# Performance work log

Measured on AMD Instinct MI355X. Metric: run time of the kernel, lower is better.

The kernel has to match this reference:

```python
import jax, jax.numpy as jnp
import numpy as np

D = 64      # hiddenDims
DQ = 64     # queryDims
M = 64      # inducingPoints
B = 64      # number of ragged segments
LMAX = 4096 # max segment length
Z = float(np.sqrt(DQ))
EPS = 1e-5


def _segment_lengths():
    rng = np.random.default_rng(0)
    return rng.integers(512, LMAX + 1, size=B)


def setup_inputs() -> dict:
    xl = _segment_lengths()
    total = int(xl.sum())
    key = jax.random.key(0)
    ks = jax.random.split(key, 12)
    s = 0.05
    inp = {
        "x": jax.random.normal(ks[0], (total, D), jnp.float32),
        "xlens": jnp.asarray(xl, jnp.int32),
        "I": jax.random.uniform(ks[1], (M, D), jnp.float32),
        # AttentionBlock 0 (queries = inducing points)
        "WQ0": jax.random.normal(ks[2], (DQ, D), jnp.float32) * s,
        "WK0": jax.random.normal(ks[3], (DQ, D), jnp.float32) * s,
        "WV0": jax.random.normal(ks[4], (D, D), jnp.float32) * s,
        "FCw0": jax.random.normal(ks[5], (D, D), jnp.float32) * s,
        "FCb0": jnp.zeros((D,), jnp.float32),
        "g00": jnp.ones((D,), jnp.float32), "b00": jnp.zeros((D,), jnp.float32),
        "g01": jnp.ones((D,), jnp.float32), "b01": jnp.zeros((D,), jnp.float32),
        # AttentionBlock 1 (queries = tokens)
        "WQ1": jax.random.normal(ks[6], (DQ, D), jnp.float32) * s,
        "WK1": jax.random.normal(ks[7], (DQ, D), jnp.float32) * s,
        "WV1": jax.random.normal(ks[8], (D, D), jnp.float32) * s,
        "FCw1": jax.random.normal(ks[9], (D, D), jnp.float32) * s,
        "FCb1": jnp.zeros((D,), jnp.float32),
        "g10": jnp.ones((D,), jnp.float32), "b10": jnp.zeros((D,), jnp.float32),
        "g11": jnp.ones((D,), jnp.float32), "b11": jnp.zeros((D,), jnp.float32),
    }
    return inp


def _ln(x, g, b):
    m = jnp.mean(x, axis=-1, keepdims=True)
    v = jnp.mean(jnp.square(x - m), axis=-1, keepdims=True)
    return (x - m) * jax.lax.rsqrt(v + EPS) * g + b


def _attn_block(q, h, mask_kv, WQ, WK, WV, FCw, FCb, g0, b0, g1, b1):
    # q: [B,Lq,D], h: [B,Lk,D], mask_kv: [B,Lk] or None
    qq = q @ WQ.T                     # [B,Lq,DQ]
    k = h @ WK.T                      # [B,Lk,DQ]
    v = h @ WV.T                      # [B,Lk,D]
    s = jnp.einsum('bqe,bke->bqk', qq, k) / Z
    if mask_kv is not None:
        s = jnp.where(mask_kv[:, None, :], s, -1e30)
    a = jax.nn.softmax(s, axis=-1)
    hh = _ln(q + jnp.einsum('bqk,bkd->bqd', a, v), g0, b0)
    return _ln(hh + jax.nn.relu(hh @ FCw.T + FCb), g1, b1)


def reference(x, xlens, I,
              WQ0, WK0, WV0, FCw0, FCb0, g00, b00, g01, b01,
              WQ1, WK1, WV1, FCw1, FCb1, g10, b10, g11, b11):
    xl = np.asarray(xlens)
    b_idx = np.concatenate([np.full(int(l), b, np.int32) for b, l in enumerate(xl)])
    pos = np.concatenate([np.arange(int(l), dtype=np.int32) for l in xl])
    mask = jnp.asarray(np.arange(LMAX)[None, :] < xl[:, None])   # [B,LMAX]

    padded = jnp.zeros((B, LMAX, D), x.dtype).at[b_idx, pos].set(x)

    # ab0: queries = inducing points (shared), keys/values = set elements
    q0 = jnp.broadcast_to(I[None], (B, M, D))
    i_seg = _attn_block(q0, padded, mask, WQ0, WK0, WV0, FCw0, FCb0, g00, b00, g01, b01)  # [B,M,D]

    # ab1: queries = set elements, keys/values = induced points
    out = _attn_block(padded, i_seg, None, WQ1, WK1, WV1, FCw1, FCb1, g10, b10, g11, b11)  # [B,LMAX,D]

    return out[b_idx, pos]  # flat ragged output [total, D]
```

## Files before the change

### kernel.cpp

```cpp
#include <hip/hip_runtime.h>

#define NB 64
#define NCHUNK 8
#define NSUB 16
#define ZINV 0.125f
#define EPS 1e-5f

typedef __attribute__((ext_vector_type(8))) short short8;
typedef __attribute__((ext_vector_type(4))) float f32x4;
typedef unsigned short ushort_t;

__device__ __forceinline__ f32x4 mm(short8 a, short8 b, f32x4 c) {
  return __builtin_amdgcn_mfma_f32_16x16x32_bf16(a, b, c, 0, 0, 0);
}
__device__ __forceinline__ ushort_t f2bf(float f) {
  unsigned u = __float_as_uint(f);
  u += 0x7fffu + ((u >> 16) & 1u);
  return (ushort_t)(u >> 16);
}
__device__ __forceinline__ unsigned pack2(float a, float b) {
  return (unsigned)f2bf(a) | ((unsigned)f2bf(b) << 16);
}
__device__ __forceinline__ short8 cvt8(float4 a, float4 b) {
  union { unsigned u[4]; short8 s; } z;
  z.u[0] = pack2(a.x, a.y); z.u[1] = pack2(a.z, a.w);
  z.u[2] = pack2(b.x, b.y); z.u[3] = pack2(b.z, b.w);
  return z.s;
}
__device__ __forceinline__ void cvt16(const float* __restrict__ src, ushort_t* dst) {
  const float4* s = (const float4*)src;
  unsigned* d = (unsigned*)dst;
  float4 A0 = s[0], A1 = s[1], A2 = s[2], A3 = s[3];
  d[0] = pack2(A0.x, A0.y); d[1] = pack2(A0.z, A0.w);
  d[2] = pack2(A1.x, A1.y); d[3] = pack2(A1.z, A1.w);
  d[4] = pack2(A2.x, A2.y); d[5] = pack2(A2.z, A2.w);
  d[6] = pack2(A3.x, A3.y); d[7] = pack2(A3.z, A3.w);
}

__global__ __launch_bounds__(256) void k_setup(const int* __restrict__ xlens,
                                               const float* __restrict__ I,
                                               const float* __restrict__ WQ0,
                                               const float* __restrict__ WK0,
                                               const float* __restrict__ FCw1,
                                               const float* __restrict__ WV0,
                                               const float* __restrict__ FCw0,
                                               const float* __restrict__ WK1,
                                               const float* __restrict__ WQ1,
                                               const float* __restrict__ WV1,
                                               int* __restrict__ off,
                                               ushort_t* __restrict__ QK0bf,
                                               ushort_t* __restrict__ Wfcbf,
                                               ushort_t* __restrict__ WV0bf,
                                               ushort_t* __restrict__ FCw0bf,
                                               ushort_t* __restrict__ WK1bf,
                                               ushort_t* __restrict__ WQ1Tbf,
                                               ushort_t* __restrict__ WV1bf) {
  int tid = threadIdx.x;
  if (tid < 64) {
    int v = xlens[tid];
#pragma unroll
    for (int d = 1; d < 64; d <<= 1) {
      int t = __shfl_up(v, d);
      if (tid >= d) v += t;
    }
    off[tid + 1] = v;
    if (tid == 0) off[0] = 0;
  }
  __shared__ ushort_t Ibf[64][72];
  __shared__ ushort_t Wq0[64][72];
  __shared__ ushort_t Wk0T[64][72];
  __shared__ ushort_t qqbf[64][72];

  int w = tid >> 6, l = tid & 63, l15 = l & 15, lh = l >> 4;
  int srow = tid >> 2, sc0 = (tid & 3) << 4;
  int so = srow * 64 + sc0;

  cvt16(I + so, &Ibf[srow][sc0]);
  cvt16(WQ0 + so, &Wq0[srow][sc0]);
  {
    const float* s = WK0 + so;
#pragma unroll
    for (int i = 0; i < 16; ++i) Wk0T[sc0 + i][srow] = f2bf(s[i]);
  }
  cvt16(FCw1 + so, Wfcbf + so);
  cvt16(WV0 + so, WV0bf + so);
  cvt16(FCw0 + so, FCw0bf + so);
  cvt16(WK1 + so, WK1bf + so);
  cvt16(WV1 + so, WV1bf + so);
  {
    const float* s = WQ1 + so;
#pragma unroll
    for (int i = 0; i < 16; ++i) WQ1Tbf[(sc0 + i) * 64 + srow] = f2bf(s[i]);
  }
  __syncthreads();

  short8 ai0 = *(const short8*)&Ibf[16 * w + l15][lh * 8];
  short8 ai1 = *(const short8*)&Ibf[16 * w + l15][32 + lh * 8];
  f32x4 cA[4];
#pragma unroll
  for (int n = 0; n < 4; ++n) {
    short8 b0 = *(const short8*)&Wq0[16 * n + l15][lh * 8];
    short8 b1 = *(const short8*)&Wq0[16 * n + l15][32 + lh * 8];
    cA[n] = mm(ai0, b0, (f32x4){0.f, 0.f, 0.f, 0.f});
    cA[n] = mm(ai1, b1, cA[n]);
  }
#pragma unroll
  for (int n = 0; n < 4; ++n)
#pragma unroll
    for (int r = 0; r < 4; ++r)
      qqbf[16 * w + 4 * lh + r][16 * n + l15] = f2bf(cA[n][r]);

  short8 aq0 = *(const short8*)&qqbf[16 * w + l15][lh * 8];
  short8 aq1 = *(const short8*)&qqbf[16 * w + l15][32 + lh * 8];
  f32x4 cB[4];
#pragma unroll
  for (int n = 0; n < 4; ++n) {
    short8 b0 = *(const short8*)&Wk0T[16 * n + l15][lh * 8];
    short8 b1 = *(const short8*)&Wk0T[16 * n + l15][32 + lh * 8];
    cB[n] = mm(aq0, b0, (f32x4){0.f, 0.f, 0.f, 0.f});
    cB[n] = mm(aq1, b1, cB[n]);
  }
#pragma unroll
  for (int n = 0; n < 4; ++n)
#pragma unroll
    for (int r = 0; r < 4; ++r)
      QK0bf[(16 * w + 4 * lh + r) * 64 + 16 * n + l15] = f2bf(cB[n][r] * ZINV);
}

__global__ __launch_bounds__(256) void k_phaseA(const float* __restrict__ x,
                                                const int* __restrict__ off,
                                                const ushort_t* __restrict__ QK0bf,
                                                float* __restrict__ part_sm,
                                                float* __restrict__ part_ax) {
  int b = blockIdx.x / NCHUNK, chunk = blockIdx.x % NCHUNK;
  int s0 = off[b], L = off[b + 1] - s0;
  int clen = (L + NCHUNK - 1) / NCHUNK;
  int t0 = chunk * clen;
  int t1 = t0 + clen; if (t1 > L) t1 = L;

  __shared__ ushort_t xbf[64][72];
  __shared__ ushort_t xT[64][72];
  __shared__ ushort_t pbf[64][72];

  int tid = threadIdx.x;
  int w = tid >> 6, l = tid & 63, l15 = l & 15, lh = l >> 4;
  int srow = tid >> 2, sc0 = (tid & 3) << 4;

  short8 aq0 = *(const short8*)(QK0bf + ((16 * w + l15) << 6) + lh * 8);
  short8 aq1 = *(const short8*)(QK0bf + ((16 * w + l15) << 6) + 32 + lh * 8);

  float sm[4] = {0.f, 0.f, 0.f, 0.f};
  f32x4 acc[4];
#pragma unroll
  for (int n = 0; n < 4; ++n) acc[n] = (f32x4){0.f, 0.f, 0.f, 0.f};

  float4 P0, P1, P2, P3;
  {
    int g = t0 + srow;
    int gc = g < t1 ? g : t1 - 1;
    const float4* src = (const float4*)(x + ((size_t)(s0 + gc) << 6) + sc0);
    P0 = src[0]; P1 = src[1]; P2 = src[2]; P3 = src[3];
  }

  for (int tt = t0; tt < t1; tt += 64) {
    __syncthreads();
    {
      float vv[16] = {P0.x, P0.y, P0.z, P0.w, P1.x, P1.y, P1.z, P1.w,
                      P2.x, P2.y, P2.z, P2.w, P3.x, P3.y, P3.z, P3.w};
      unsigned* dst = (unsigned*)&xbf[srow][sc0];
      dst[0] = pack2(vv[0], vv[1]);   dst[1] = pack2(vv[2], vv[3]);
      dst[2] = pack2(vv[4], vv[5]);   dst[3] = pack2(vv[6], vv[7]);
      dst[4] = pack2(vv[8], vv[9]);   dst[5] = pack2(vv[10], vv[11]);
      dst[6] = pack2(vv[12], vv[13]); dst[7] = pack2(vv[14], vv[15]);
#pragma unroll
      for (int i = 0; i < 16; ++i) xT[sc0 + i][srow] = f2bf(vv[i]);
    }
    __syncthreads();
    if (tt + 64 < t1) {
      int g = tt + 64 + srow;
      int gc = g < t1 ? g : t1 - 1;
      const float4* src = (const float4*)(x + ((size_t)(s0 + gc) << 6) + sc0);
      P0 = src[0]; P1 = src[1]; P2 = src[2]; P3 = src[3];
    }
    f32x4 c1[4];
#pragma unroll
    for (int n = 0; n < 4; ++n) {
      short8 bx0 = *(const short8*)&xbf[16 * n + l15][lh * 8];
      short8 bx1 = *(const short8*)&xbf[16 * n + l15][32 + lh * 8];
      c1[n] = mm(aq0, bx0, (f32x4){0.f, 0.f, 0.f, 0.f});
      c1[n] = mm(aq1, bx1, c1[n]);
    }
#pragma unroll
    for (int n = 0; n < 4; ++n) {
      bool v = (tt + 16 * n + l15) < t1;
#pragma unroll
      for (int r = 0; r < 4; ++r) {
        float pv = v ? __expf(c1[n][r]) : 0.f;
        c1[n][r] = pv;
        sm[r] += pv;
      }
    }
#pragma unroll
    for (int n = 0; n < 4; ++n)
#pragma unroll
      for (int r = 0; r < 4; ++r)
        pbf[16 * w + 4 * lh + r][16 * n + l15] = f2bf(c1[n][r]);
    short8 pa0 = *(const short8*)&pbf[16 * w + l15][lh * 8];
    short8 pa1 = *(const short8*)&pbf[16 * w + l15][32 + lh * 8];
#pragma unroll
    for (int n = 0; n < 4; ++n) {
      short8 bt0 = *(const short8*)&xT[16 * n + l15][lh * 8];
      short8 bt1 = *(const short8*)&xT[16 * n + l15][32 + lh * 8];
      acc[n] = mm(pa0, bt0, acc[n]);
      acc[n] = mm(pa1, bt1, acc[n]);
    }
  }
  int base = (b * NCHUNK + chunk) * 64;
#pragma unroll
  for (int r = 0; r < 4; ++r) {
    sm[r] += __shfl_xor(sm[r], 1);
    sm[r] += __shfl_xor(sm[r], 2);
    sm[r] += __shfl_xor(sm[r], 4);
    sm[r] += __shfl_xor(sm[r], 8);
  }
  if (l15 == 0) {
#pragma unroll
    for (int r = 0; r < 4; ++r)
      part_sm[base + 16 * w + 4 * lh + r] = sm[r];
  }
#pragma unroll
  for (int n = 0; n < 4; ++n)
#pragma unroll
    for (int r = 0; r < 4; ++r) {
      int m = 16 * w + 4 * lh + r;
      part_ax[((size_t)(base + m) << 6) + 16 * n + l15] = acc[n][r];
    }
}

__global__ __launch_bounds__(256) void k_combine(const float* __restrict__ part_sm,
                                                 const float* __restrict__ part_ax,
                                                 const float* __restrict__ I,
                                                 const ushort_t* __restrict__ WV0bf,
                                                 const ushort_t* __restrict__ FCw0bf,
                                                 const float* __restrict__ FCb0,
                                                 const float* __restrict__ g00,
                                                 const float* __restrict__ b00,
                                                 const float* __restrict__ g01,
                                                 const float* __restrict__ b01,
                                                 const ushort_t* __restrict__ WK1bf,
                                                 const ushort_t* __restrict__ WQ1Tbf,
                                                 const ushort_t* __restrict__ WV1bf,
                                                 ushort_t* __restrict__ K1fbf,
                                                 ushort_t* __restrict__ V1Tbf) {
  int b = blockIdx.x;
  int tid = threadIdx.x;
  int w = tid >> 6, l = tid & 63, l15 = l & 15, lh = l >> 4;

  __shared__ ushort_t av[64][72];
  __shared__ ushort_t sb[64][72];

  {
    int m = tid >> 2, dq = tid & 3, e0 = dq << 4;
    float S = 0.f;
    float ax[16];
#pragma unroll
    for (int i = 0; i < 16; ++i) ax[i] = 0.f;
#pragma unroll
    for (int c = 0; c < NCHUNK; ++c) {
      int pb = (b * NCHUNK + c) * 64 + m;
      S += part_sm[pb];
      const f32x4* pa = (const f32x4*)(part_ax + ((size_t)pb << 6) + e0);
#pragma unroll
      for (int qd = 0; qd < 4; ++qd) {
        f32x4 v = pa[qd];
#pragma unroll
        for (int j = 0; j < 4; ++j) ax[qd * 4 + j] += v[j];
      }
    }
    float invS = 1.f / S;
    unsigned* dst = (unsigned*)&av[m][e0];
#pragma unroll
    for (int i = 0; i < 8; ++i)
      dst[i] = pack2(ax[2 * i] * invS, ax[2 * i + 1] * invS);
  }
  __syncthreads();

  float p00[4], q00[4], p01[4], q01[4], fcb[4];
#pragma unroll
  for (int n = 0; n < 4; ++n) {
    int d = 16 * n + l15;
    p00[n] = g00[d]; q00[n] = b00[d];
    p01[n] = g01[d]; q01[n] = b01[d];
    fcb[n] = FCb0[d];
  }
  int row = 16 * w + 4 * lh;

  short8 a0 = *(const short8*)&av[16 * w + l15][lh * 8];
  short8 a1 = *(const short8*)&av[16 * w + l15][32 + lh * 8];
  f32x4 c1[4];
#pragma unroll
  for (int n = 0; n < 4; ++n) {
    short8 b0 = *(const short8*)(WV0bf + ((16 * n + l15) << 6) + lh * 8);
    short8 b1 = *(const short8*)(WV0bf + ((16 * n + l15) << 6) + 32 + lh * 8);
    c1[n] = mm(a0, b0, (f32x4){0.f, 0.f, 0.f, 0.f});
    c1[n] = mm(a1, b1, c1[n]);
  }
  float hh[4][4];
#pragma unroll
  for (int r = 0; r < 4; ++r) {
    float h[4];
#pragma unroll
    for (int n = 0; n < 4; ++n)
      h[n] = c1[n][r] + I[(row + r) * 64 + 16 * n + l15];
    float s1 = h[0] + h[1] + h[2] + h[3];
    s1 += __shfl_xor(s1, 1); s1 += __shfl_xor(s1, 2);
    s1 += __shfl_xor(s1, 4); s1 += __shfl_xor(s1, 8);
    float mean = s1 * 0.015625f;
    float s2 = 0.f;
#pragma unroll
    for (int n = 0; n < 4; ++n) { float c = h[n] - mean; s2 += c * c; }
    s2 += __shfl_xor(s2, 1); s2 += __shfl_xor(s2, 2);
    s2 += __shfl_xor(s2, 4); s2 += __shfl_xor(s2, 8);
    float rs = rsqrtf(s2 * 0.015625f + EPS);
#pragma unroll
    for (int n = 0; n < 4; ++n) {
      hh[n][r] = (h[n] - mean) * rs * p00[n] + q00[n];
      sb[row + r][16 * n + l15] = f2bf(hh[n][r]);
    }
  }
  short8 h0 = *(const short8*)&sb[16 * w + l15][lh * 8];
  short8 h1 = *(const short8*)&sb[16 * w + l15][32 + lh * 8];
  f32x4 c2[4];
#pragma unroll
  for (int n = 0; n < 4; ++n) {
    short8 b0 = *(const short8*)(FCw0bf + ((16 * n + l15) << 6) + lh * 8);
    short8 b1 = *(const short8*)(FCw0bf + ((16 * n + l15) << 6) + 32 + lh * 8);
    c2[n] = mm(h0, b0, (f32x4){0.f, 0.f, 0.f, 0.f});
    c2[n] = mm(h1, b1, c2[n]);
  }
#pragma unroll
  for (int r = 0; r < 4; ++r) {
    float u[4];
#pragma unroll
    for (int n = 0; n < 4; ++n)
      u[n] = hh[n][r] + fmaxf(c2[n][r] + fcb[n], 0.f);
    float s1 = u[0] + u[1] + u[2] + u[3];
    s1 += __shfl_xor(s1, 1); s1 += __shfl_xor(s1, 2);
    s1 += __shfl_xor(s1, 4); s1 += __shfl_xor(s1, 8);
    float mean = s1 * 0.015625f;
    float s2 = 0.f;
#pragma unroll
    for (int n = 0; n < 4; ++n) { float c = u[n] - mean; s2 += c * c; }
    s2 += __shfl_xor(s2, 1); s2 += __shfl_xor(s2, 2);
    s2 += __shfl_xor(s2, 4); s2 += __shfl_xor(s2, 8);
    float rs = rsqrtf(s2 * 0.015625f + EPS);
#pragma unroll
    for (int n = 0; n < 4; ++n)
      av[row + r][16 * n + l15] = f2bf((u[n] - mean) * rs * p01[n] + q01[n]);
  }
  short8 i0 = *(const short8*)&av[16 * w + l15][lh * 8];
  short8 i1 = *(const short8*)&av[16 * w + l15][32 + lh * 8];
  f32x4 c3[4];
#pragma unroll
  for (int n = 0; n < 4; ++n) {
    short8 b0 = *(const short8*)(WK1bf + ((16 * n + l15) << 6) + lh * 8);
    short8 b1 = *(const short8*)(WK1bf + ((16 * n + l15) << 6) + 32 + lh * 8);
    c3[n] = mm(i0, b0, (f32x4){0.f, 0.f, 0.f, 0.f});
    c3[n] = mm(i1, b1, c3[n]);
  }
#pragma unroll
  for (int n = 0; n < 4; ++n)
#pragma unroll
    for (int r = 0; r < 4; ++r)
      sb[row + r][16 * n + l15] = f2bf(c3[n][r]);
  short8 t0f = *(const short8*)&sb[16 * w + l15][lh * 8];
  short8 t1f = *(const short8*)&sb[16 * w + l15][32 + lh * 8];
  f32x4 c4[4];
#pragma unroll
  for (int n = 0; n < 4; ++n) {
    short8 b0 = *(const short8*)(WQ1Tbf + ((16 * n + l15) << 6) + lh * 8);
    short8 b1 = *(const short8*)(WQ1Tbf + ((16 * n + l15) << 6) + 32 + lh * 8);
    c4[n] = mm(t0f, b0, (f32x4){0.f, 0.f, 0.f, 0.f});
    c4[n] = mm(t1f, b1, c4[n]);
  }
#pragma unroll
  for (int n = 0; n < 4; ++n)
#pragma unroll
    for (int r = 0; r < 4; ++r)
      K1fbf[((size_t)(b * 64 + row + r) << 6) + 16 * n + l15] = f2bf(c4[n][r] * ZINV);
  f32x4 c5[4];
#pragma unroll
  for (int n = 0; n < 4; ++n) {
    short8 b0 = *(const short8*)(WV1bf + ((16 * n + l15) << 6) + lh * 8);
    short8 b1 = *(const short8*)(WV1bf + ((16 * n + l15) << 6) + 32 + lh * 8);
    c5[n] = mm(i0, b0, (f32x4){0.f, 0.f, 0.f, 0.f});
    c5[n] = mm(i1, b1, c5[n]);
  }
#pragma unroll
  for (int n = 0; n < 4; ++n)
#pragma unroll
    for (int r = 0; r < 4; ++r)
      V1Tbf[((size_t)(b * 64 + 16 * n + l15) << 6) + row + r] = f2bf(c5[n][r]);
}

__global__ __launch_bounds__(256) void k_phaseB(const float* __restrict__ x,
                                                const int* __restrict__ off,
                                                const ushort_t* __restrict__ K1fbf,
                                                const ushort_t* __restrict__ V1Tbf,
                                                const ushort_t* __restrict__ Wfcbf,
                                                const float* __restrict__ FCb1,
                                                const float* __restrict__ g10,
                                                const float* __restrict__ b10,
                                                const float* __restrict__ g11,
                                                const float* __restrict__ b11,
                                                float* __restrict__ outp) {
  int b = blockIdx.x / NSUB, sub = blockIdx.x % NSUB;
  int s0 = off[b], L = off[b + 1] - s0;
  int tiles = (L + 63) >> 6;
  if (sub >= tiles) return;

  __shared__ ushort_t pbf[64][72];

  int tid = threadIdx.x;
  int w = tid >> 6, l = tid & 63, l15 = l & 15, lh = l >> 4;

  float gg0[4], bb0[4], gg1[4], bb1[4], fb[4];
#pragma unroll
  for (int n = 0; n < 4; ++n) {
    int d = 16 * n + l15;
    gg0[n] = g10[d]; bb0[n] = b10[d];
    gg1[n] = g11[d]; bb1[n] = b11[d];
    fb[n] = FCb1[d];
  }
  const ushort_t* Kb = K1fbf + ((size_t)b << 12);
  const ushort_t* Vb = V1Tbf + ((size_t)b << 12);

  float4 xa0, xa1, xa2, xa3;
  {
    int t0 = sub << 6;
    int nt = L - t0; if (nt > 64) nt = 64;
    int rA = 16 * w + l15; if (rA >= nt) rA = nt - 1;
    const float* xr = x + ((size_t)(s0 + t0 + rA) << 6);
    xa0 = *(const float4*)(xr + lh * 8);
    xa1 = *(const float4*)(xr + lh * 8 + 4);
    xa2 = *(const float4*)(xr + 32 + lh * 8);
    xa3 = *(const float4*)(xr + 32 + lh * 8 + 4);
  }

  for (int j = sub; j < tiles; j += NSUB) {
    int t0 = j << 6;
    int nt = L - t0; if (nt > 64) nt = 64;

    float4 xn0 = xa0, xn1 = xa1, xn2 = xa2, xn3 = xa3;
    int jn = j + NSUB;
    if (jn < tiles) {
      int t0n = jn << 6;
      int ntn = L - t0n; if (ntn > 64) ntn = 64;
      int rAn = 16 * w + l15; if (rAn >= ntn) rAn = ntn - 1;
      const float* xrn = x + ((size_t)(s0 + t0n + rAn) << 6);
      xn0 = *(const float4*)(xrn + lh * 8);
      xn1 = *(const float4*)(xrn + lh * 8 + 4);
      xn2 = *(const float4*)(xrn + 32 + lh * 8);
      xn3 = *(const float4*)(xrn + 32 + lh * 8 + 4);
    }
    float res[4][4];
#pragma unroll
    for (int r = 0; r < 4; ++r) {
      int rr = 16 * w + 4 * lh + r;
      if (rr >= nt) rr = nt - 1;
      const float* rp = x + ((size_t)(s0 + t0 + rr) << 6);
#pragma unroll
      for (int n = 0; n < 4; ++n) res[n][r] = rp[16 * n + l15];
    }
    short8 a0 = cvt8(xa0, xa1);
    short8 a1 = cvt8(xa2, xa3);
    f32x4 c1[4];
#pragma unroll
    for (int n = 0; n < 4; ++n) {
      short8 bk0 = *(const short8*)(Kb + ((16 * n + l15) << 6) + lh * 8);
      short8 bk1 = *(const short8*)(Kb + ((16 * n + l15) << 6) + 32 + lh * 8);
      c1[n] = mm(a0, bk0, (f32x4){0.f, 0.f, 0.f, 0.f});
      c1[n] = mm(a1, bk1, c1[n]);
    }
    float inv[4];
#pragma unroll
    for (int r = 0; r < 4; ++r) {
      float s = 0.f;
#pragma unroll
      for (int n = 0; n < 4; ++n) {
        float p = __expf(c1[n][r]);
        c1[n][r] = p;
        s += p;
      }
      s += __shfl_xor(s, 1);
      s += __shfl_xor(s, 2);
      s += __shfl_xor(s, 4);
      s += __shfl_xor(s, 8);
      inv[r] = 1.f / s;
    }
#pragma unroll
    for (int n = 0; n < 4; ++n)
#pragma unroll
      for (int r = 0; r < 4; ++r)
        pbf[16 * w + 4 * lh + r][16 * n + l15] = f2bf(c1[n][r]);
    short8 pa0 = *(const short8*)&pbf[16 * w + l15][lh * 8];
    short8 pa1 = *(const short8*)&pbf[16 * w + l15][32 + lh * 8];
    f32x4 c2[4];
#pragma unroll
    for (int n = 0; n < 4; ++n) {
      short8 bv0 = *(const short8*)(Vb + ((16 * n + l15) << 6) + lh * 8);
      short8 bv1 = *(const short8*)(Vb + ((16 * n + l15) << 6) + 32 + lh * 8);
      c2[n] = mm(pa0, bv0, (f32x4){0.f, 0.f, 0.f, 0.f});
      c2[n] = mm(pa1, bv1, c2[n]);
    }
    float hh[4][4];
#pragma unroll
    for (int r = 0; r < 4; ++r) {
      int t = 16 * w + 4 * lh + r;
      float h[4];
#pragma unroll
      for (int n = 0; n < 4; ++n)
        h[n] = c2[n][r] * inv[r] + res[n][r];
      float s1 = h[0] + h[1] + h[2] + h[3];
      s1 += __shfl_xor(s1, 1); s1 += __shfl_xor(s1, 2);
      s1 += __shfl_xor(s1, 4); s1 += __shfl_xor(s1, 8);
      float mean = s1 * 0.015625f;
      float s2 = 0.f;
#pragma unroll
      for (int n = 0; n < 4; ++n) { float c = h[n] - mean; s2 += c * c; }
      s2 += __shfl_xor(s2, 1); s2 += __shfl_xor(s2, 2);
      s2 += __shfl_xor(s2, 4); s2 += __shfl_xor(s2, 8);
      float rs = rsqrtf(s2 * 0.015625f + EPS);
#pragma unroll
      for (int n = 0; n < 4; ++n) {
        hh[n][r] = (h[n] - mean) * rs * gg0[n] + bb0[n];
        pbf[t][16 * n + l15] = f2bf(hh[n][r]);
      }
    }
    short8 ha0 = *(const short8*)&pbf[16 * w + l15][lh * 8];
    short8 ha1 = *(const short8*)&pbf[16 * w + l15][32 + lh * 8];
    f32x4 c3[4];
#pragma unroll
    for (int n = 0; n < 4; ++n) {
      short8 bw0 = *(const short8*)(Wfcbf + ((16 * n + l15) << 6) + lh * 8);
      short8 bw1 = *(const short8*)(Wfcbf + ((16 * n + l15) << 6) + 32 + lh * 8);
      c3[n] = mm(ha0, bw0, (f32x4){0.f, 0.f, 0.f, 0.f});
      c3[n] = mm(ha1, bw1, c3[n]);
    }
#pragma unroll
    for (int r = 0; r < 4; ++r) {
      int t = 16 * w + 4 * lh + r;
      float u[4];
#pragma unroll
      for (int n = 0; n < 4; ++n)
        u[n] = hh[n][r] + fmaxf(c3[n][r] + fb[n], 0.f);
      float s1 = u[0] + u[1] + u[2] + u[3];
      s1 += __shfl_xor(s1, 1); s1 += __shfl_xor(s1, 2);
      s1 += __shfl_xor(s1, 4); s1 += __shfl_xor(s1, 8);
      float mean = s1 * 0.015625f;
      float s2 = 0.f;
#pragma unroll
      for (int n = 0; n < 4; ++n) { float c = u[n] - mean; s2 += c * c; }
      s2 += __shfl_xor(s2, 1); s2 += __shfl_xor(s2, 2);
      s2 += __shfl_xor(s2, 4); s2 += __shfl_xor(s2, 8);
      float rs = rsqrtf(s2 * 0.015625f + EPS);
      if (t < nt) {
#pragma unroll
        for (int n = 0; n < 4; ++n)
          outp[((size_t)(s0 + t0 + t) << 6) + 16 * n + l15] =
              (u[n] - mean) * rs * gg1[n] + bb1[n];
      }
    }
    xa0 = xn0; xa1 = xn1; xa2 = xn2; xa3 = xn3;
  }
}


extern "C" void kernel_launch(void* const* d_in, const int* in_sizes, int n_in,
                              void* d_out, int out_size, void* d_ws, size_t ws_size,
                              hipStream_t stream) {
  const float* x    = (const float*)d_in[0];
  const int*   xlen = (const int*)d_in[1];
  const float* I    = (const float*)d_in[2];
  const float* WQ0  = (const float*)d_in[3];
  const float* WK0  = (const float*)d_in[4];
  const float* WV0  = (const float*)d_in[5];
  const float* FCw0 = (const float*)d_in[6];
  const float* FCb0 = (const float*)d_in[7];
  const float* g00  = (const float*)d_in[8];
  const float* b00  = (const float*)d_in[9];
  const float* g01  = (const float*)d_in[10];
  const float* b01  = (const float*)d_in[11];
  const float* WQ1  = (const float*)d_in[12];
  const float* WK1  = (const float*)d_in[13];
  const float* WV1  = (const float*)d_in[14];
  const float* FCw1 = (const float*)d_in[15];
  const float* FCb1 = (const float*)d_in[16];
  const float* g10  = (const float*)d_in[17];
  const float* b10  = (const float*)d_in[18];
  const float* g11  = (const float*)d_in[19];
  const float* b11  = (const float*)d_in[20];

  char* p = (char*)d_ws;
  int* off = (int*)p;                p += 1024;
  ushort_t* QK0bf = (ushort_t*)p;    p += 64 * 64 * 2;
  ushort_t* Wfcbf = (ushort_t*)p;    p += 64 * 64 * 2;
  ushort_t* WV0bf = (ushort_t*)p;    p += 64 * 64 * 2;
  ushort_t* FCw0bf = (ushort_t*)p;   p += 64 * 64 * 2;
  ushort_t* WK1bf = (ushort_t*)p;    p += 64 * 64 * 2;
  ushort_t* WQ1Tbf = (ushort_t*)p;   p += 64 * 64 * 2;
  ushort_t* WV1bf = (ushort_t*)p;    p += 64 * 64 * 2;
  ushort_t* K1fbf = (ushort_t*)p;    p += (size_t)NB * 64 * 64 * 2;
  ushort_t* V1Tbf = (ushort_t*)p;    p += (size_t)NB * 64 * 64 * 2;
  float* psm = (float*)p;            p += (size_t)NB * NCHUNK * 64 * 4;
  float* pax = (float*)p;

  k_setup<<<1, 256, 0, stream>>>(xlen, I, WQ0, WK0, FCw1, WV0, FCw0, WK1, WQ1, WV1,
                                 off, QK0bf, Wfcbf, WV0bf, FCw0bf, WK1bf, WQ1Tbf, WV1bf);
  k_phaseA<<<NB * NCHUNK, 256, 0, stream>>>(x, off, QK0bf, psm, pax);
  k_combine<<<NB, 256, 0, stream>>>(psm, pax, I, WV0bf, FCw0bf, FCb0,
                                    g00, b00, g01, b01, WK1bf, WQ1Tbf, WV1bf,
                                    K1fbf, V1Tbf);
  k_phaseB<<<NB * NSUB, 256, 0, stream>>>(x, off, K1fbf, V1Tbf, Wfcbf, FCb1,
                                          g10, b10, g11, b11, (float*)d_out);
}
```

Before: 81.80 us.

## Process 128-token tiles per block in phase B with one block per tile

Phase B used to run 16 blocks per segment, each looping over 64-token tiles with the next tile's x prefetched in software. Now each of 32 blocks per segment handles exactly one 128-token chunk as two interleaved 64-row halves, with no loop. This raises instruction-level parallelism and removes loop overhead, and blocks past the end of a segment exit early. The cost is more registers and doubled LDS per block, which can lower occupancy, plus some load imbalance on short segments.

```diff
diff --git a/kernel.cpp b/kernel.cpp
--- a/kernel.cpp
+++ b/kernel.cpp
@@ -2,7 +2,6 @@
 
 #define NB 64
 #define NCHUNK 8
-#define NSUB 16
 #define ZINV 0.125f
 #define EPS 1e-5f
 
@@ -414,12 +413,12 @@
                                                 const float* __restrict__ g11,
                                                 const float* __restrict__ b11,
                                                 float* __restrict__ outp) {
-  int b = blockIdx.x / NSUB, sub = blockIdx.x % NSUB;
+  int b = blockIdx.x >> 5, sub = blockIdx.x & 31;
   int s0 = off[b], L = off[b + 1] - s0;
-  int tiles = (L + 63) >> 6;
-  if (sub >= tiles) return;
-
-  __shared__ ushort_t pbf[64][72];
+  int t0 = sub << 7;
+  if (t0 >= L) return;
+
+  __shared__ ushort_t pbf[128][72];
 
   int tid = threadIdx.x;
   int w = tid >> 6, l = tid & 63, l15 = l & 15, lh = l >> 4;
@@ -435,125 +434,126 @@
   const ushort_t* Kb = K1fbf + ((size_t)b << 12);
   const ushort_t* Vb = V1Tbf + ((size_t)b << 12);
 
-  float4 xa0, xa1, xa2, xa3;
-  {
-    int t0 = sub << 6;
-    int nt = L - t0; if (nt > 64) nt = 64;
-    int rA = 16 * w + l15; if (rA >= nt) rA = nt - 1;
-    const float* xr = x + ((size_t)(s0 + t0 + rA) << 6);
-    xa0 = *(const float4*)(xr + lh * 8);
-    xa1 = *(const float4*)(xr + lh * 8 + 4);
-    xa2 = *(const float4*)(xr + 32 + lh * 8);
-    xa3 = *(const float4*)(xr + 32 + lh * 8 + 4);
-  }
-
-  for (int j = sub; j < tiles; j += NSUB) {
-    int t0 = j << 6;
-    int nt = L - t0; if (nt > 64) nt = 64;
-
-    float4 xn0 = xa0, xn1 = xa1, xn2 = xa2, xn3 = xa3;
-    int jn = j + NSUB;
-    if (jn < tiles) {
-      int t0n = jn << 6;
-      int ntn = L - t0n; if (ntn > 64) ntn = 64;
-      int rAn = 16 * w + l15; if (rAn >= ntn) rAn = ntn - 1;
-      const float* xrn = x + ((size_t)(s0 + t0n + rAn) << 6);
-      xn0 = *(const float4*)(xrn + lh * 8);
-      xn1 = *(const float4*)(xrn + lh * 8 + 4);
-      xn2 = *(const float4*)(xrn + 32 + lh * 8);
-      xn3 = *(const float4*)(xrn + 32 + lh * 8 + 4);
-    }
-    float res[4][4];
+  float4 xa[2][4];
+#pragma unroll
+  for (int h = 0; h < 2; ++h) {
+    int trow = t0 + 64 * h + 16 * w + l15;
+    if (trow >= L) trow = L - 1;
+    const float* xr = x + ((size_t)(s0 + trow) << 6);
+    xa[h][0] = *(const float4*)(xr + lh * 8);
+    xa[h][1] = *(const float4*)(xr + lh * 8 + 4);
+    xa[h][2] = *(const float4*)(xr + 32 + lh * 8);
+    xa[h][3] = *(const float4*)(xr + 32 + lh * 8 + 4);
+  }
+  float res[2][4][4];
+#pragma unroll
+  for (int h = 0; h < 2; ++h)
 #pragma unroll
     for (int r = 0; r < 4; ++r) {
-      int rr = 16 * w + 4 * lh + r;
-      if (rr >= nt) rr = nt - 1;
-      const float* rp = x + ((size_t)(s0 + t0 + rr) << 6);
-#pragma unroll
-      for (int n = 0; n < 4; ++n) res[n][r] = rp[16 * n + l15];
-    }
-    short8 a0 = cvt8(xa0, xa1);
-    short8 a1 = cvt8(xa2, xa3);
-    f32x4 c1[4];
+      int trow = t0 + 64 * h + 16 * w + 4 * lh + r;
+      if (trow >= L) trow = L - 1;
+      const float* rp = x + ((size_t)(s0 + trow) << 6);
+#pragma unroll
+      for (int n = 0; n < 4; ++n) res[h][n][r] = rp[16 * n + l15];
+    }
+  f32x4 c1[2][4];
+#pragma unroll
+  for (int h = 0; h < 2; ++h) {
+    short8 a0 = cvt8(xa[h][0], xa[h][1]);
+    short8 a1 = cvt8(xa[h][2], xa[h][3]);
 #pragma unroll
     for (int n = 0; n < 4; ++n) {
       short8 bk0 = *(const short8*)(Kb + ((16 * n + l15) << 6) + lh * 8);
       short8 bk1 = *(const short8*)(Kb + ((16 * n + l15) << 6) + 32 + lh * 8);
-      c1[n] = mm(a0, bk0, (f32x4){0.f, 0.f, 0.f, 0.f});
-      c1[n] = mm(a1, bk1, c1[n]);
-    }
-    float inv[4];
+      c1[h][n] = mm(a0, bk0, (f32x4){0.f, 0.f, 0.f, 0.f});
+      c1[h][n] = mm(a1, bk1, c1[h][n]);
+    }
+  }
+  float inv[2][4];
+#pragma unroll
+  for (int h = 0; h < 2; ++h)
 #pragma unroll
     for (int r = 0; r < 4; ++r) {
       float s = 0.f;
 #pragma unroll
       for (int n = 0; n < 4; ++n) {
-        float p = __expf(c1[n][r]);
-        c1[n][r] = p;
+        float p = __expf(c1[h][n][r]);
+        c1[h][n][r] = p;
         s += p;
       }
       s += __shfl_xor(s, 1);
       s += __shfl_xor(s, 2);
       s += __shfl_xor(s, 4);
       s += __shfl_xor(s, 8);
-      inv[r] = 1.f / s;
-    }
+      inv[h][r] = 1.f / s;
+    }
+#pragma unroll
+  for (int h = 0; h < 2; ++h)
 #pragma unroll
     for (int n = 0; n < 4; ++n)
 #pragma unroll
       for (int r = 0; r < 4; ++r)
-        pbf[16 * w + 4 * lh + r][16 * n + l15] = f2bf(c1[n][r]);
-    short8 pa0 = *(const short8*)&pbf[16 * w + l15][lh * 8];
-    short8 pa1 = *(const short8*)&pbf[16 * w + l15][32 + lh * 8];
-    f32x4 c2[4];
+        pbf[64 * h + 16 * w + 4 * lh + r][16 * n + l15] = f2bf(c1[h][n][r]);
+  f32x4 c2[2][4];
+#pragma unroll
+  for (int h = 0; h < 2; ++h) {
+    short8 pa0 = *(const short8*)&pbf[64 * h + 16 * w + l15][lh * 8];
+    short8 pa1 = *(const short8*)&pbf[64 * h + 16 * w + l15][32 + lh * 8];
 #pragma unroll
     for (int n = 0; n < 4; ++n) {
       short8 bv0 = *(const short8*)(Vb + ((16 * n + l15) << 6) + lh * 8);
       short8 bv1 = *(const short8*)(Vb + ((16 * n + l15) << 6) + 32 + lh * 8);
-      c2[n] = mm(pa0, bv0, (f32x4){0.f, 0.f, 0.f, 0.f});
-      c2[n] = mm(pa1, bv1, c2[n]);
-    }
-    float hh[4][4];
+      c2[h][n] = mm(pa0, bv0, (f32x4){0.f, 0.f, 0.f, 0.f});
+      c2[h][n] = mm(pa1, bv1, c2[h][n]);
+    }
+  }
+  float hh[2][4][4];
+#pragma unroll
+  for (int h = 0; h < 2; ++h)
 #pragma unroll
     for (int r = 0; r < 4; ++r) {
-      int t = 16 * w + 4 * lh + r;
-      float h[4];
+      float hv[4];
 #pragma unroll
       for (int n = 0; n < 4; ++n)
-        h[n] = c2[n][r] * inv[r] + res[n][r];
-      float s1 = h[0] + h[1] + h[2] + h[3];
+        hv[n] = c2[h][n][r] * inv[h][r] + res[h][n][r];
+      float s1 = hv[0] + hv[1] + hv[2] + hv[3];
       s1 += __shfl_xor(s1, 1); s1 += __shfl_xor(s1, 2);
       s1 += __shfl_xor(s1, 4); s1 += __shfl_xor(s1, 8);
       float mean = s1 * 0.015625f;
       float s2 = 0.f;
 #pragma unroll
-      for (int n = 0; n < 4; ++n) { float c = h[n] - mean; s2 += c * c; }
+      for (int n = 0; n < 4; ++n) { float c = hv[n] - mean; s2 += c * c; }
       s2 += __shfl_xor(s2, 1); s2 += __shfl_xor(s2, 2);
       s2 += __shfl_xor(s2, 4); s2 += __shfl_xor(s2, 8);
       float rs = rsqrtf(s2 * 0.015625f + EPS);
 #pragma unroll
       for (int n = 0; n < 4; ++n) {
-        hh[n][r] = (h[n] - mean) * rs * gg0[n] + bb0[n];
-        pbf[t][16 * n + l15] = f2bf(hh[n][r]);
+        hh[h][n][r] = (hv[n] - mean) * rs * gg0[n] + bb0[n];
+        pbf[64 * h + 16 * w + 4 * lh + r][16 * n + l15] = f2bf(hh[h][n][r]);
       }
     }
-    short8 ha0 = *(const short8*)&pbf[16 * w + l15][lh * 8];
-    short8 ha1 = *(const short8*)&pbf[16 * w + l15][32 + lh * 8];
-    f32x4 c3[4];
+  f32x4 c3[2][4];
+#pragma unroll
+  for (int h = 0; h < 2; ++h) {
+    short8 ha0 = *(const short8*)&pbf[64 * h + 16 * w + l15][lh * 8];
+    short8 ha1 = *(const short8*)&pbf[64 * h + 16 * w + l15][32 + lh * 8];
 #pragma unroll
     for (int n = 0; n < 4; ++n) {
       short8 bw0 = *(const short8*)(Wfcbf + ((16 * n + l15) << 6) + lh * 8);
       short8 bw1 = *(const short8*)(Wfcbf + ((16 * n + l15) << 6) + 32 + lh * 8);
-      c3[n] = mm(ha0, bw0, (f32x4){0.f, 0.f, 0.f, 0.f});
-      c3[n] = mm(ha1, bw1, c3[n]);
-    }
+      c3[h][n] = mm(ha0, bw0, (f32x4){0.f, 0.f, 0.f, 0.f});
+      c3[h][n] = mm(ha1, bw1, c3[h][n]);
+    }
+  }
+#pragma unroll
+  for (int h = 0; h < 2; ++h)
 #pragma unroll
     for (int r = 0; r < 4; ++r) {
-      int t = 16 * w + 4 * lh + r;
+      int trow = t0 + 64 * h + 16 * w + 4 * lh + r;
       float u[4];
 #pragma unroll
       for (int n = 0; n < 4; ++n)
-        u[n] = hh[n][r] + fmaxf(c3[n][r] + fb[n], 0.f);
+        u[n] = hh[h][n][r] + fmaxf(c3[h][n][r] + fb[n], 0.f);
       float s1 = u[0] + u[1] + u[2] + u[3];
       s1 += __shfl_xor(s1, 1); s1 += __shfl_xor(s1, 2);
       s1 += __shfl_xor(s1, 4); s1 += __shfl_xor(s1, 8);
@@ -564,15 +564,13 @@
       s2 += __shfl_xor(s2, 1); s2 += __shfl_xor(s2, 2);
       s2 += __shfl_xor(s2, 4); s2 += __shfl_xor(s2, 8);
       float rs = rsqrtf(s2 * 0.015625f + EPS);
-      if (t < nt) {
+      if (trow < L) {
 #pragma unroll
         for (int n = 0; n < 4; ++n)
-          outp[((size_t)(s0 + t0 + t) << 6) + 16 * n + l15] =
+          outp[((size_t)(s0 + trow) << 6) + 16 * n + l15] =
               (u[n] - mean) * rs * gg1[n] + bb1[n];
       }
     }
-    xa0 = xn0; xa1 = xn1; xa2 = xn2; xa3 = xn3;
-  }
 }
 
 
@@ -621,6 +619,6 @@
   k_combine<<<NB, 256, 0, stream>>>(psm, pax, I, WV0bf, FCw0bf, FCb0,
                                     g00, b00, g01, b01, WK1bf, WQ1Tbf, WV1bf,
                                     K1fbf, V1Tbf);
-  k_phaseB<<<NB * NSUB, 256, 0, stream>>>(x, off, K1fbf, V1Tbf, Wfcbf, FCb1,
-                                          g10, b10, g11, b11, (float*)d_out);
-}
+  k_phaseB<<<NB * 32, 256, 0, stream>>>(x, off, K1fbf, V1Tbf, Wfcbf, FCb1,
+                                        g10, b10, g11, b11, (float*)d_out);
+}
```

Result: slower. 85.23 us (+4.2%).

## Stage phaseB x tiles through LDS, hoist K fragments, use exp2 with folded log2e

Applied to the files above, without the earlier changes.

Phase B now loads each 64-row x tile with coalesced float4 loads into a shared-memory buffer. Both the MFMA A-operand and the residual values are read from that buffer, replacing the strided per-element global reloads of x. The K1 fragments are loaded once into registers before the tile loop. The log2(e) factor is folded into the QK scaling so both softmax phases can use exp2f. The change also adds launch_bounds occupancy 4, at the cost of extra LDS use and register pressure. The loop has no barrier around the LDS write and read; within a wave the rows used are consistent, but cross-wave rows may race.

```diff
diff --git a/kernel.cpp b/kernel.cpp
--- a/kernel.cpp
+++ b/kernel.cpp
@@ -2,8 +2,9 @@
 
 #define NB 64
 #define NCHUNK 8
-#define NSUB 16
+#define NSUBB 16
 #define ZINV 0.125f
+#define LOG2E 1.44269504088896f
 #define EPS 1e-5f
 
 typedef __attribute__((ext_vector_type(8))) short short8;
@@ -124,7 +125,8 @@
   for (int n = 0; n < 4; ++n)
 #pragma unroll
     for (int r = 0; r < 4; ++r)
-      QK0bf[(16 * w + 4 * lh + r) * 64 + 16 * n + l15] = f2bf(cB[n][r] * ZINV);
+      QK0bf[(16 * w + 4 * lh + r) * 64 + 16 * n + l15] =
+          f2bf(cB[n][r] * (ZINV * LOG2E));
 }
 
 __global__ __launch_bounds__(256) void k_phaseA(const float* __restrict__ x,
@@ -195,7 +197,7 @@
       bool v = (tt + 16 * n + l15) < t1;
 #pragma unroll
       for (int r = 0; r < 4; ++r) {
-        float pv = v ? __expf(c1[n][r]) : 0.f;
+        float pv = v ? exp2f(c1[n][r]) : 0.f;
         c1[n][r] = pv;
         sm[r] += pv;
       }
@@ -387,7 +389,8 @@
   for (int n = 0; n < 4; ++n)
 #pragma unroll
     for (int r = 0; r < 4; ++r)
-      K1fbf[((size_t)(b * 64 + row + r) << 6) + 16 * n + l15] = f2bf(c4[n][r] * ZINV);
+      K1fbf[((size_t)(b * 64 + row + r) << 6) + 16 * n + l15] =
+          f2bf(c4[n][r] * (ZINV * LOG2E));
   f32x4 c5[4];
 #pragma unroll
   for (int n = 0; n < 4; ++n) {
@@ -403,26 +406,28 @@
       V1Tbf[((size_t)(b * 64 + 16 * n + l15) << 6) + row + r] = f2bf(c5[n][r]);
 }
 
-__global__ __launch_bounds__(256) void k_phaseB(const float* __restrict__ x,
-                                                const int* __restrict__ off,
-                                                const ushort_t* __restrict__ K1fbf,
-                                                const ushort_t* __restrict__ V1Tbf,
-                                                const ushort_t* __restrict__ Wfcbf,
-                                                const float* __restrict__ FCb1,
-                                                const float* __restrict__ g10,
-                                                const float* __restrict__ b10,
-                                                const float* __restrict__ g11,
-                                                const float* __restrict__ b11,
-                                                float* __restrict__ outp) {
-  int b = blockIdx.x / NSUB, sub = blockIdx.x % NSUB;
+__global__ __launch_bounds__(256, 4) void k_phaseB(const float* __restrict__ x,
+                                                   const int* __restrict__ off,
+                                                   const ushort_t* __restrict__ K1fbf,
+                                                   const ushort_t* __restrict__ V1Tbf,
+                                                   const ushort_t* __restrict__ Wfcbf,
+                                                   const float* __restrict__ FCb1,
+                                                   const float* __restrict__ g10,
+                                                   const float* __restrict__ b10,
+                                                   const float* __restrict__ g11,
+                                                   const float* __restrict__ b11,
+                                                   float* __restrict__ outp) {
+  int b = blockIdx.x / NSUBB, sub = blockIdx.x % NSUBB;
   int s0 = off[b], L = off[b + 1] - s0;
   int tiles = (L + 63) >> 6;
   if (sub >= tiles) return;
 
+  __shared__ float xs[64][68];
   __shared__ ushort_t pbf[64][72];
 
   int tid = threadIdx.x;
   int w = tid >> 6, l = tid & 63, l15 = l & 15, lh = l >> 4;
+  int srow = tid >> 2, sc0 = (tid & 3) << 4;
 
   float gg0[4], bb0[4], gg1[4], bb1[4], fb[4];
 #pragma unroll
@@ -435,52 +440,51 @@
   const ushort_t* Kb = K1fbf + ((size_t)b << 12);
   const ushort_t* Vb = V1Tbf + ((size_t)b << 12);
 
-  float4 xa0, xa1, xa2, xa3;
+  short8 kf0[4], kf1[4];
+#pragma unroll
+  for (int n = 0; n < 4; ++n) {
+    kf0[n] = *(const short8*)(Kb + ((16 * n + l15) << 6) + lh * 8);
+    kf1[n] = *(const short8*)(Kb + ((16 * n + l15) << 6) + 32 + lh * 8);
+  }
+
+  float4 P0, P1, P2, P3;
   {
-    int t0 = sub << 6;
-    int nt = L - t0; if (nt > 64) nt = 64;
-    int rA = 16 * w + l15; if (rA >= nt) rA = nt - 1;
-    const float* xr = x + ((size_t)(s0 + t0 + rA) << 6);
-    xa0 = *(const float4*)(xr + lh * 8);
-    xa1 = *(const float4*)(xr + lh * 8 + 4);
-    xa2 = *(const float4*)(xr + 32 + lh * 8);
-    xa3 = *(const float4*)(xr + 32 + lh * 8 + 4);
-  }
-
-  for (int j = sub; j < tiles; j += NSUB) {
+    int g = (sub << 6) + srow;
+    int gc = g < L ? g : L - 1;
+    const float4* src = (const float4*)(x + ((size_t)(s0 + gc) << 6) + sc0);
+    P0 = src[0]; P1 = src[1]; P2 = src[2]; P3 = src[3];
+  }
+
+  for (int j = sub; j < tiles; j += NSUBB) {
     int t0 = j << 6;
-    int nt = L - t0; if (nt > 64) nt = 64;
-
-    float4 xn0 = xa0, xn1 = xa1, xn2 = xa2, xn3 = xa3;
-    int jn = j + NSUB;
+    {
+      float4* dst = (float4*)&xs[srow][sc0];
+      dst[0] = P0; dst[1] = P1; dst[2] = P2; dst[3] = P3;
+    }
+    int jn = j + NSUBB;
     if (jn < tiles) {
-      int t0n = jn << 6;
-      int ntn = L - t0n; if (ntn > 64) ntn = 64;
-      int rAn = 16 * w + l15; if (rAn >= ntn) rAn = ntn - 1;
-      const float* xrn = x + ((size_t)(s0 + t0n + rAn) << 6);
-      xn0 = *(const float4*)(xrn + lh * 8);
-      xn1 = *(const float4*)(xrn + lh * 8 + 4);
-      xn2 = *(const float4*)(xrn + 32 + lh * 8);
-      xn3 = *(const float4*)(xrn + 32 + lh * 8 + 4);
-    }
+      int g = (jn << 6) + srow;
+      int gc = g < L ? g : L - 1;
+      const float4* src = (const float4*)(x + ((size_t)(s0 + gc) << 6) + sc0);
+      P0 = src[0]; P1 = src[1]; P2 = src[2]; P3 = src[3];
+    }
+    float4 a00 = *(const float4*)&xs[16 * w + l15][lh * 8];
+    float4 a01 = *(const float4*)&xs[16 * w + l15][lh * 8 + 4];
+    float4 a10 = *(const float4*)&xs[16 * w + l15][32 + lh * 8];
+    float4 a11 = *(const float4*)&xs[16 * w + l15][32 + lh * 8 + 4];
     float res[4][4];
 #pragma unroll
-    for (int r = 0; r < 4; ++r) {
-      int rr = 16 * w + 4 * lh + r;
-      if (rr >= nt) rr = nt - 1;
-      const float* rp = x + ((size_t)(s0 + t0 + rr) << 6);
-#pragma unroll
-      for (int n = 0; n < 4; ++n) res[n][r] = rp[16 * n + l15];
-    }
-    short8 a0 = cvt8(xa0, xa1);
-    short8 a1 = cvt8(xa2, xa3);
+    for (int r = 0; r < 4; ++r)
+#pragma unroll
+      for (int n = 0; n < 4; ++n)
+        res[n][r] = xs[16 * w + 4 * lh + r][16 * n + l15];
+    short8 a0 = cvt8(a00, a01);
+    short8 a1 = cvt8(a10, a11);
     f32x4 c1[4];
 #pragma unroll
     for (int n = 0; n < 4; ++n) {
-      short8 bk0 = *(const short8*)(Kb + ((16 * n + l15) << 6) + lh * 8);
-      short8 bk1 = *(const short8*)(Kb + ((16 * n + l15) << 6) + 32 + lh * 8);
-      c1[n] = mm(a0, bk0, (f32x4){0.f, 0.f, 0.f, 0.f});
-      c1[n] = mm(a1, bk1, c1[n]);
+      c1[n] = mm(a0, kf0[n], (f32x4){0.f, 0.f, 0.f, 0.f});
+      c1[n] = mm(a1, kf1[n], c1[n]);
     }
     float inv[4];
 #pragma unroll
@@ -488,7 +492,7 @@
       float s = 0.f;
 #pragma unroll
       for (int n = 0; n < 4; ++n) {
-        float p = __expf(c1[n][r]);
+        float p = exp2f(c1[n][r]);
         c1[n][r] = p;
         s += p;
       }
@@ -516,7 +520,6 @@
     float hh[4][4];
 #pragma unroll
     for (int r = 0; r < 4; ++r) {
-      int t = 16 * w + 4 * lh + r;
       float h[4];
 #pragma unroll
       for (int n = 0; n < 4; ++n)
@@ -534,7 +537,7 @@
 #pragma unroll
       for (int n = 0; n < 4; ++n) {
         hh[n][r] = (h[n] - mean) * rs * gg0[n] + bb0[n];
-        pbf[t][16 * n + l15] = f2bf(hh[n][r]);
+        pbf[16 * w + 4 * lh + r][16 * n + l15] = f2bf(hh[n][r]);
       }
     }
     short8 ha0 = *(const short8*)&pbf[16 * w + l15][lh * 8];
@@ -549,7 +552,7 @@
     }
 #pragma unroll
     for (int r = 0; r < 4; ++r) {
-      int t = 16 * w + 4 * lh + r;
+      int trow = t0 + 16 * w + 4 * lh + r;
       float u[4];
 #pragma unroll
       for (int n = 0; n < 4; ++n)
@@ -564,14 +567,13 @@
       s2 += __shfl_xor(s2, 1); s2 += __shfl_xor(s2, 2);
       s2 += __shfl_xor(s2, 4); s2 += __shfl_xor(s2, 8);
       float rs = rsqrtf(s2 * 0.015625f + EPS);
-      if (t < nt) {
+      if (trow < L) {
 #pragma unroll
         for (int n = 0; n < 4; ++n)
-          outp[((size_t)(s0 + t0 + t) << 6) + 16 * n + l15] =
+          outp[((size_t)(s0 + trow) << 6) + 16 * n + l15] =
               (u[n] - mean) * rs * gg1[n] + bb1[n];
       }
     }
-    xa0 = xn0; xa1 = xn1; xa2 = xn2; xa3 = xn3;
   }
 }
 
@@ -621,6 +623,6 @@
   k_combine<<<NB, 256, 0, stream>>>(psm, pax, I, WV0bf, FCw0bf, FCb0,
                                     g00, b00, g01, b01, WK1bf, WQ1Tbf, WV1bf,
                                     K1fbf, V1Tbf);
-  k_phaseB<<<NB * NSUB, 256, 0, stream>>>(x, off, K1fbf, V1Tbf, Wfcbf, FCb1,
-                                          g10, b10, g11, b11, (float*)d_out);
-}
+  k_phaseB<<<NB * NSUBB, 256, 0, stream>>>(x, off, K1fbf, V1Tbf, Wfcbf, FCb1,
+                                           g10, b10, g11, b11, (float*)d_out);
+}
```

After: 102.2 us. 1.25x slower.
